# Kernel tuning notes

Hardware: AMD Instinct MI355X
Metric: run time of the kernel (lower is better)

Reference implementation:

```python
import jax, jax.numpy as jnp
import numpy as np

NUM_ITERATIONS = 3


def _squash(s):
    # s: [B, J, S]. Faithful to the torch code: squash norm is computed over
    # dim=2 of s_j [B,1,J,S,1], i.e. the num_unit (J) axis here.
    mag_sq = jnp.sum(s * s, axis=1, keepdims=True)  # [B, 1, S]
    mag = jnp.sqrt(mag_sq)
    return s * (mag_sq / (1.0 + mag_sq) / mag)


def setup_inputs() -> dict:
    key = jax.random.key(0)
    k1, k2 = jax.random.split(key)
    B, U, C, J, S = 128, 8, 2048, 32, 16
    x = jax.random.normal(k1, (B, U, C), dtype=jnp.float32)
    W = jax.random.normal(k2, (1, C, J, S, U), dtype=jnp.float32)
    return {"x": x, "W": W}


def reference(x, W):
    # x: [B, in_unit, in_channel]; W: [1, C, J, S, U]
    xt = jnp.swapaxes(x, 1, 2)          # [B, C, U]
    Wc = W[0]                           # [C, J, S, U]
    # u_hat = W @ x (per input capsule c, output capsule j): [B, C, J, S]
    u_hat = jnp.einsum('cjsu,bcu->bcjs', Wc, xt)
    B, C, J, _ = u_hat.shape
    b = jnp.zeros((C, J), dtype=u_hat.dtype)
    v = None
    for _ in range(NUM_ITERATIONS):
        # legacy F.softmax on 4D [1,C,J,1] defaults to dim=1 -> over C
        c = jax.nn.softmax(b, axis=0)                      # [C, J]
        s = jnp.einsum('cj,bcjs->bjs', c, u_hat)           # [B, J, S]
        v = _squash(s)                                     # [B, J, S]
        # agreement, mean over batch (keepdim handled by shape [C,J])
        b = b + jnp.einsum('bcjs,bjs->cj', u_hat, v) / B
    return v[..., None]  # [B, num_unit, unit_size, 1] == v_j.squeeze(1)
```

## Files before the change

kernel.cpp:

```cpp
#include <hip/hip_runtime.h>
#include <hip/hip_bf16.h>

#define BB 128
#define UU 8
#define CC 2048
#define JJ 32
#define SS 16

typedef unsigned int u32;
typedef unsigned short u16;
typedef __attribute__((ext_vector_type(8))) short bf16x8;
typedef __attribute__((ext_vector_type(4))) float f32x4;

__device__ __forceinline__ float bflo(u32 p) { return __uint_as_float(p << 16); }
__device__ __forceinline__ float bfhi(u32 p) { return __uint_as_float(p & 0xffff0000u); }
__device__ __forceinline__ u32 f2b(float f) {
    u32 bits = __float_as_uint(f);
    u32 r = bits + 0x7fffu + ((bits >> 16) & 1u);
    return r >> 16;
}
__device__ __forceinline__ u32 pack2(float a, float b) { return f2b(a) | (f2b(b) << 16); }
__device__ __forceinline__ uint4 scale4(uint4 p, float cw) {
    uint4 o;
    o.x = pack2(bflo(p.x) * cw, bfhi(p.x) * cw);
    o.y = pack2(bflo(p.y) * cw, bfhi(p.y) * cw);
    o.z = pack2(bflo(p.z) * cw, bfhi(p.z) * cw);
    o.w = pack2(bflo(p.w) * cw, bfhi(p.w) * cw);
    return o;
}

__global__ __launch_bounds__(256) void k_prep(const float* __restrict__ x,
                                              const float* __restrict__ W,
                                              u16* __restrict__ xA,
                                              u16* __restrict__ xB,
                                              u16* __restrict__ Wn,
                                              float* __restrict__ bbp) {
    __shared__ uint4 ldsu[16][129];
    int blk = blockIdx.x, t = threadIdx.x;
    if (blk < 1024) {
        int b = blk >> 3;
        int c = (blk & 7) * 256 + t;
        const float* xf = x + (size_t)b * UU * CC;
        float v[8];
#pragma unroll
        for (int u = 0; u < 8; ++u) v[u] = xf[u * CC + c];
        uint4 p;
        p.x = pack2(v[0], v[1]);
        p.y = pack2(v[2], v[3]);
        p.z = pack2(v[4], v[5]);
        p.w = pack2(v[6], v[7]);
        ((uint4*)xA)[(size_t)b * CC + c] = p;
    } else if (blk < 2048) {
        int bb2 = blk - 1024;
        int u = bb2 >> 7, c0 = (bb2 & 127) * 16;
        float* ldsf = (float*)ldsu;
        int b = t >> 1, h = t & 1;
        const float4* x4 = (const float4*)(x + ((size_t)b * UU + u) * CC + c0);
        float4 lo = x4[h * 2], hi = x4[h * 2 + 1];
        ldsf[(h * 8 + 0) * 129 + b] = lo.x; ldsf[(h * 8 + 1) * 129 + b] = lo.y;
        ldsf[(h * 8 + 2) * 129 + b] = lo.z; ldsf[(h * 8 + 3) * 129 + b] = lo.w;
        ldsf[(h * 8 + 4) * 129 + b] = hi.x; ldsf[(h * 8 + 5) * 129 + b] = hi.y;
        ldsf[(h * 8 + 6) * 129 + b] = hi.z; ldsf[(h * 8 + 7) * 129 + b] = hi.w;
        __syncthreads();
        int ci = t >> 4, k8 = t & 15;
        const float* r = ldsf + ci * 129 + k8 * 8;
        uint4 p;
        p.x = pack2(r[0], r[1]);
        p.y = pack2(r[2], r[3]);
        p.z = pack2(r[4], r[5]);
        p.w = pack2(r[6], r[7]);
        ((uint4*)xB)[((size_t)u * CC + c0 + ci) * 16 + k8] = p;
    } else if (blk < 2560) {
        int bb2 = blk - 2048;
        int ct = bb2 & 127, nt = bb2 >> 7;
        int c0 = ct * 16, n0 = nt * 128;
        const float4* Wf = (const float4*)W;
        for (int q = t; q < 2048; q += 256) {
            int ci = q >> 7, ni = q & 127;
            size_t widx = (size_t)(c0 + ci) * 512 + n0 + ni;
            float4 lo = Wf[2 * widx], hi = Wf[2 * widx + 1];
            uint4 o;
            o.x = pack2(lo.x, lo.y);
            o.y = pack2(lo.z, lo.w);
            o.z = pack2(hi.x, hi.y);
            o.w = pack2(hi.z, hi.w);
            ldsu[ci][ni] = o;
        }
        __syncthreads();
        for (int q = t; q < 2048; q += 256) {
            int ni = q >> 4, ci = q & 15;
            ((uint4*)Wn)[(size_t)(n0 + ni) * 2048 + c0 + ci] = ldsu[ci][ni];
        }
    } else {
        int base = (blk - 2560) * 4096 + t;
#pragma unroll
        for (int r = 0; r < 16; ++r) bbp[base + r * 256] = 0.f;
    }
}

__global__ __launch_bounds__(256) void k_softmax(const float* __restrict__ bbp,
                                                 float* __restrict__ ccp) {
    int j = blockIdx.x, t = threadIdx.x;
    __shared__ float red[4];
    __shared__ float bcast[2];
    const float* row = bbp + j * CC;
    float m = -1e30f;
    for (int c = t; c < CC; c += 256) m = fmaxf(m, row[c]);
#pragma unroll
    for (int o = 32; o > 0; o >>= 1) m = fmaxf(m, __shfl_down(m, o, 64));
    if ((t & 63) == 0) red[t >> 6] = m;
    __syncthreads();
    if (t == 0) bcast[0] = fmaxf(fmaxf(red[0], red[1]), fmaxf(red[2], red[3]));
    __syncthreads();
    float mm = bcast[0];
    float ssum = 0.f;
    for (int c = t; c < CC; c += 256) ssum += expf(row[c] - mm);
#pragma unroll
    for (int o = 32; o > 0; o >>= 1) ssum += __shfl_down(ssum, o, 64);
    if ((t & 63) == 0) red[t >> 6] = ssum;
    __syncthreads();
    if (t == 0) bcast[1] = red[0] + red[1] + red[2] + red[3];
    __syncthreads();
    float inv = 1.0f / bcast[1];
    for (int c = t; c < CC; c += 256) ccp[j * CC + c] = expf(row[c] - mm) * inv;
}

__global__ __launch_bounds__(256) void k_gemmA(const u16* __restrict__ xA,
                                               const u16* __restrict__ Wn,
                                               const float* __restrict__ ccp,
                                               int use_cc,
                                               float* __restrict__ spart) {
    const bf16x8* A8 = (const bf16x8*)xA;
    const uint4* B4 = (const uint4*)Wn;
    int t = threadIdx.x;
    int w = t >> 6, lane = t & 63;
    int gw = blockIdx.x * 4 + w;
    int sl = gw >> 6, rest = gw & 63;
    int mg = rest & 3, ng = rest >> 2;
    int ln = lane & 15, quad = lane >> 4;
    int rowA0 = (mg * 32 + ln) * 2048;
    int rowA1 = rowA0 + 16 * 2048;
    int rowB0 = (ng * 32 + ln) * 2048;
    int rowB1 = rowB0 + 16 * 2048;
    const float* cc0 = ccp + (2 * ng) * CC;
    const float* cc1 = cc0 + CC;
    int kk = sl * 64 + quad;
    f32x4 acc00 = {0.f, 0.f, 0.f, 0.f};
    f32x4 acc01 = acc00, acc10 = acc00, acc11 = acc00;
#pragma unroll 4
    for (int step = 0; step < 16; ++step) {
        bf16x8 a0 = A8[rowA0 + kk];
        bf16x8 a1 = A8[rowA1 + kk];
        uint4 wb0 = B4[rowB0 + kk];
        uint4 wb1 = B4[rowB1 + kk];
        if (use_cc) {
            float cw0 = cc0[kk];
            float cw1 = cc1[kk];
            wb0 = scale4(wb0, cw0);
            wb1 = scale4(wb1, cw1);
        }
        bf16x8 b0 = __builtin_bit_cast(bf16x8, wb0);
        bf16x8 b1 = __builtin_bit_cast(bf16x8, wb1);
        kk += 4;
        acc00 = __builtin_amdgcn_mfma_f32_16x16x32_bf16(a0, b0, acc00, 0, 0, 0);
        acc01 = __builtin_amdgcn_mfma_f32_16x16x32_bf16(a0, b1, acc01, 0, 0, 0);
        acc10 = __builtin_amdgcn_mfma_f32_16x16x32_bf16(a1, b0, acc10, 0, 0, 0);
        acc11 = __builtin_amdgcn_mfma_f32_16x16x32_bf16(a1, b1, acc11, 0, 0, 0);
    }
    float* outp = spart + sl * (BB * JJ * SS);
    int b0r = mg * 32 + quad * 4;
    int n00 = ng * 32 + ln;
#pragma unroll
    for (int r = 0; r < 4; ++r) {
        int b = b0r + r;
        outp[b * 512 + n00] = acc00[r];
        outp[b * 512 + n00 + 16] = acc01[r];
        outp[(b + 16) * 512 + n00] = acc10[r];
        outp[(b + 16) * 512 + n00 + 16] = acc11[r];
    }
}

__global__ __launch_bounds__(512) void k_rsq(const float* __restrict__ spart,
                                             u16* __restrict__ vB,
                                             float* __restrict__ out,
                                             float scale_pre, int write_out) {
    __shared__ float s[512];
    __shared__ float sc[16];
    int b = blockIdx.x, n = threadIdx.x;
    float v = 0.f;
#pragma unroll
    for (int sl = 0; sl < 32; ++sl) v += spart[sl * (BB * JJ * SS) + b * 512 + n];
    v *= scale_pre;
    s[n] = v;
    __syncthreads();
    if (n < 16) {
        float msq = 0.f;
#pragma unroll
        for (int jj = 0; jj < 32; ++jj) {
            float tv = s[jj * 16 + n];
            msq = fmaf(tv, tv, msq);
        }
        sc[n] = msq / ((1.f + msq) * sqrtf(fmaxf(msq, 1e-30f)));
    }
    __syncthreads();
    float vv = s[n] * sc[n & 15];
    vB[n * BB + b] = (u16)f2b(vv);
    if (write_out) out[b * 512 + n] = vv;
}

__global__ __launch_bounds__(256) void k_gemmB1(const u16* __restrict__ vB,
                                                const u16* __restrict__ xB,
                                                u16* __restrict__ G) {
    const bf16x8* A8 = (const bf16x8*)vB;
    const bf16x8* B8 = (const bf16x8*)xB;
    int t = threadIdx.x;
    int w = t >> 6, lane = t & 63;
    int gw = blockIdx.x * 4 + w;
    int u = gw >> 10, rest = gw & 1023;
    int n0 = (rest & 15) * 32, c0 = (rest >> 4) * 32;
    int ln = lane & 15, quad = lane >> 4;
    bf16x8 av[2][4], bx[2][4];
#pragma unroll
    for (int mt = 0; mt < 2; ++mt)
#pragma unroll
        for (int st = 0; st < 4; ++st)
            av[mt][st] = A8[(n0 + mt * 16 + ln) * 16 + quad + 4 * st];
#pragma unroll
    for (int ct = 0; ct < 2; ++ct)
#pragma unroll
        for (int st = 0; st < 4; ++st)
            bx[ct][st] = B8[((size_t)u * CC + c0 + ct * 16 + ln) * 16 + quad + 4 * st];
    f32x4 acc[2][2];
    acc[0][0] = {0.f, 0.f, 0.f, 0.f};
    acc[0][1] = acc[0][0]; acc[1][0] = acc[0][0]; acc[1][1] = acc[0][0];
#pragma unroll
    for (int st = 0; st < 4; ++st)
#pragma unroll
        for (int mt = 0; mt < 2; ++mt)
#pragma unroll
            for (int ct = 0; ct < 2; ++ct)
                acc[mt][ct] = __builtin_amdgcn_mfma_f32_16x16x32_bf16(
                    av[mt][st], bx[ct][st], acc[mt][ct], 0, 0, 0);
#pragma unroll
    for (int mt = 0; mt < 2; ++mt)
#pragma unroll
        for (int ct = 0; ct < 2; ++ct)
#pragma unroll
            for (int r = 0; r < 4; ++r) {
                int n = n0 + mt * 16 + quad * 4 + r;
                int c = c0 + ct * 16 + ln;
                G[((size_t)u * 512 + n) * 2048 + c] = (u16)f2b(acc[mt][ct][r]);
            }
}

__global__ __launch_bounds__(256) void k_bbsum(const u16* __restrict__ Wn,
                                               const u16* __restrict__ G,
                                               float* __restrict__ bbp) {
    __shared__ u32 Wlds[128][33];
    __shared__ float red[4][128];
    int j = blockIdx.x & 31;
    int c0 = ((blockIdx.x >> 5) & 15) * 128;
    int sh = blockIdx.x >> 9;
    int t = threadIdx.x;
    const uint4* Wn4 = (const uint4*)Wn;
#pragma unroll
    for (int it = 0; it < 4; ++it) {
        int q = t + it * 256;
        int ci = q & 127, s = q >> 7;
        uint4 p = Wn4[(size_t)(j * 16 + sh * 8 + s) * 2048 + c0 + ci];
        Wlds[ci][s * 4 + 0] = p.x;
        Wlds[ci][s * 4 + 1] = p.y;
        Wlds[ci][s * 4 + 2] = p.z;
        Wlds[ci][s * 4 + 3] = p.w;
    }
    __syncthreads();
    int w = t >> 6, cp = t & 63;
    const u32* G32 = (const u32*)G;
    float acc0 = 0.f, acc1 = 0.f;
    int u0 = 2 * w;
#pragma unroll
    for (int s = 0; s < 8; ++s) {
        u32 wl = Wlds[2 * cp][s * 4 + w];
        u32 wh = Wlds[2 * cp + 1][s * 4 + w];
        int n = j * 16 + sh * 8 + s;
        u32 g0 = G32[((size_t)u0 * 512 + n) * 1024 + (c0 >> 1) + cp];
        u32 g1 = G32[((size_t)(u0 + 1) * 512 + n) * 1024 + (c0 >> 1) + cp];
        acc0 = fmaf(bflo(wl), bflo(g0), acc0);
        acc0 = fmaf(bfhi(wl), bflo(g1), acc0);
        acc1 = fmaf(bflo(wh), bfhi(g0), acc1);
        acc1 = fmaf(bfhi(wh), bfhi(g1), acc1);
    }
    red[w][2 * cp] = acc0;
    red[w][2 * cp + 1] = acc1;
    __syncthreads();
    if (t < 128) {
        float sum = red[0][t] + red[1][t] + red[2][t] + red[3][t];
        atomicAdd(&bbp[j * CC + c0 + t], sum * (1.0f / BB));
    }
}

extern "C" void kernel_launch(void* const* d_in, const int* in_sizes, int n_in,
                              void* d_out, int out_size, void* d_ws, size_t ws_size,
                              hipStream_t stream) {
    const float* x = (const float*)d_in[0];
    const float* W = (const float*)d_in[1];
    if (in_sizes[0] == CC * JJ * SS * UU) {
        x = (const float*)d_in[1];
        W = (const float*)d_in[0];
    }
    float* out = (float*)d_out;

    char* ws = (char*)d_ws;
    u16* G = (u16*)ws;
    u16* xA = (u16*)(ws + (16u << 20));
    u16* xB = (u16*)(ws + (20u << 20));
    u16* Wn = (u16*)(ws + (24u << 20));
    float* spart = (float*)(ws + (40u << 20));
    size_t b48 = (size_t)48u << 20;
    u16* vB = (u16*)(ws + b48);
    float* bbp = (float*)(ws + b48 + 131072);
    float* ccp = (float*)(ws + b48 + 393216);

    k_prep<<<2576, 256, 0, stream>>>(x, W, xA, xB, Wn, bbp);

    for (int it = 0; it < 3; ++it) {
        if (it > 0) k_softmax<<<32, 256, 0, stream>>>(bbp, ccp);
        k_gemmA<<<512, 256, 0, stream>>>(xA, Wn, ccp, it > 0 ? 1 : 0, spart);
        k_rsq<<<128, 512, 0, stream>>>(spart, vB, out,
                                       it == 0 ? (1.0f / 2048.0f) : 1.0f,
                                       it == 2 ? 1 : 0);
        if (it < 2) {
            k_gemmB1<<<2048, 256, 0, stream>>>(vB, xB, G);
            k_bbsum<<<1024, 256, 0, stream>>>(Wn, G, bbp);
        }
    }
}
```

Baseline: 215.4 us.

## Fuse agreement GEMM with W-weighted reduction, drop G intermediate buffer

Merges the bf16 GEMM that produced the G intermediate [U,512,2048] with the bbsum kernel that multiplied G by W and reduced it. The MFMA accumulators are now multiplied by the matching W element inside the GEMM kernel, reduced across quads with shuffles, and atomically added into the logits. This removes a 16 MB round trip through global memory and one launch per iteration. In exchange it issues many more global atomics (one per u per (j,c)), does uncached 16-byte W loads to use only 2 bytes of each, and drops the rounding of G to bf16.

Result: no change. 212.8 us (-1.2%).

```diff
diff --git a/kernel.cpp b/kernel.cpp
--- a/kernel.cpp
+++ b/kernel.cpp
@@ -208,16 +208,19 @@
     if (write_out) out[b * 512 + n] = vv;
 }
 
-__global__ __launch_bounds__(256) void k_gemmB1(const u16* __restrict__ vB,
+__global__ __launch_bounds__(256) void k_gemmBf(const u16* __restrict__ vB,
                                                 const u16* __restrict__ xB,
-                                                u16* __restrict__ G) {
+                                                const u16* __restrict__ Wn,
+                                                float* __restrict__ bbp) {
     const bf16x8* A8 = (const bf16x8*)vB;
     const bf16x8* B8 = (const bf16x8*)xB;
+    const uint4* Wn4 = (const uint4*)Wn;
     int t = threadIdx.x;
     int w = t >> 6, lane = t & 63;
     int gw = blockIdx.x * 4 + w;
     int u = gw >> 10, rest = gw & 1023;
-    int n0 = (rest & 15) * 32, c0 = (rest >> 4) * 32;
+    int nt = rest & 15, c0 = (rest >> 4) * 32;
+    int n0 = nt * 32;
     int ln = lane & 15, quad = lane >> 4;
     bf16x8 av[2][4], bx[2][4];
 #pragma unroll
@@ -242,60 +245,26 @@
                 acc[mt][ct] = __builtin_amdgcn_mfma_f32_16x16x32_bf16(
                     av[mt][st], bx[ct][st], acc[mt][ct], 0, 0, 0);
 #pragma unroll
-    for (int mt = 0; mt < 2; ++mt)
-#pragma unroll
-        for (int ct = 0; ct < 2; ++ct)
+    for (int mt = 0; mt < 2; ++mt) {
+        int j = 2 * nt + mt;
+#pragma unroll
+        for (int ct = 0; ct < 2; ++ct) {
+            int c = c0 + ct * 16 + ln;
+            float val = 0.f;
 #pragma unroll
             for (int r = 0; r < 4; ++r) {
                 int n = n0 + mt * 16 + quad * 4 + r;
-                int c = c0 + ct * 16 + ln;
-                G[((size_t)u * 512 + n) * 2048 + c] = (u16)f2b(acc[mt][ct][r]);
+                uint4 wp = Wn4[(size_t)n * 2048 + c];
+                u32 warr[4] = {wp.x, wp.y, wp.z, wp.w};
+                u32 ww = warr[u >> 1];
+                float wv = (u & 1) ? bfhi(ww) : bflo(ww);
+                val = fmaf(acc[mt][ct][r], wv, val);
             }
-}
-
-__global__ __launch_bounds__(256) void k_bbsum(const u16* __restrict__ Wn,
-                                               const u16* __restrict__ G,
-                                               float* __restrict__ bbp) {
-    __shared__ u32 Wlds[128][33];
-    __shared__ float red[4][128];
-    int j = blockIdx.x & 31;
-    int c0 = ((blockIdx.x >> 5) & 15) * 128;
-    int sh = blockIdx.x >> 9;
-    int t = threadIdx.x;
-    const uint4* Wn4 = (const uint4*)Wn;
-#pragma unroll
-    for (int it = 0; it < 4; ++it) {
-        int q = t + it * 256;
-        int ci = q & 127, s = q >> 7;
-        uint4 p = Wn4[(size_t)(j * 16 + sh * 8 + s) * 2048 + c0 + ci];
-        Wlds[ci][s * 4 + 0] = p.x;
-        Wlds[ci][s * 4 + 1] = p.y;
-        Wlds[ci][s * 4 + 2] = p.z;
-        Wlds[ci][s * 4 + 3] = p.w;
-    }
-    __syncthreads();
-    int w = t >> 6, cp = t & 63;
-    const u32* G32 = (const u32*)G;
-    float acc0 = 0.f, acc1 = 0.f;
-    int u0 = 2 * w;
-#pragma unroll
-    for (int s = 0; s < 8; ++s) {
-        u32 wl = Wlds[2 * cp][s * 4 + w];
-        u32 wh = Wlds[2 * cp + 1][s * 4 + w];
-        int n = j * 16 + sh * 8 + s;
-        u32 g0 = G32[((size_t)u0 * 512 + n) * 1024 + (c0 >> 1) + cp];
-        u32 g1 = G32[((size_t)(u0 + 1) * 512 + n) * 1024 + (c0 >> 1) + cp];
-        acc0 = fmaf(bflo(wl), bflo(g0), acc0);
-        acc0 = fmaf(bfhi(wl), bflo(g1), acc0);
-        acc1 = fmaf(bflo(wh), bfhi(g0), acc1);
-        acc1 = fmaf(bfhi(wh), bfhi(g1), acc1);
-    }
-    red[w][2 * cp] = acc0;
-    red[w][2 * cp + 1] = acc1;
-    __syncthreads();
-    if (t < 128) {
-        float sum = red[0][t] + red[1][t] + red[2][t] + red[3][t];
-        atomicAdd(&bbp[j * CC + c0 + t], sum * (1.0f / BB));
+            val += __shfl_xor(val, 16, 64);
+            val += __shfl_xor(val, 32, 64);
+            if (quad == 0)
+                atomicAdd(&bbp[j * CC + c], val * (1.0f / BB));
+        }
     }
 }
 
@@ -311,7 +280,6 @@
     float* out = (float*)d_out;
 
     char* ws = (char*)d_ws;
-    u16* G = (u16*)ws;
     u16* xA = (u16*)(ws + (16u << 20));
     u16* xB = (u16*)(ws + (20u << 20));
     u16* Wn = (u16*)(ws + (24u << 20));
@@ -329,9 +297,6 @@
         k_rsq<<<128, 512, 0, stream>>>(spart, vB, out,
                                        it == 0 ? (1.0f / 2048.0f) : 1.0f,
                                        it == 2 ? 1 : 0);
-        if (it < 2) {
-            k_gemmB1<<<2048, 256, 0, stream>>>(vB, xB, G);
-            k_bbsum<<<1024, 256, 0, stream>>>(Wn, G, bbp);
-        }
-    }
-}
+        if (it < 2) k_gemmBf<<<2048, 256, 0, stream>>>(vB, xB, Wn, bbp);
+    }
+}
```
